# Optimization experiments

Hardware: AMD Instinct MI355X
Metric: run time of the kernel (lower is better)

The kernel has to match this reference:

```python
import jax, jax.numpy as jnp
import numpy as np

NUM_EMBEDDINGS = 1024
EMBEDDING_DIM = 64
COMMITMENT_COST = 0.25


def setup_inputs() -> dict:
    key = jax.random.key(0)
    k_x, k_cb = jax.random.split(key)
    x = jax.random.normal(k_x, (16, EMBEDDING_DIM, 64, 64), dtype=jnp.float32)
    # nn.Embedding weight init: uniform(-1/K, 1/K)
    codebook = jax.random.uniform(
        k_cb, (NUM_EMBEDDINGS, EMBEDDING_DIM), dtype=jnp.float32,
        minval=-1.0 / NUM_EMBEDDINGS, maxval=1.0 / NUM_EMBEDDINGS)
    return {"x": x, "codebook": codebook}


def reference(x, codebook):
    sg = jax.lax.stop_gradient
    # NCHW -> NHWC
    inputs = jnp.transpose(x, (0, 2, 3, 1))  # [B,H,W,D]
    in_shape = inputs.shape
    flat = inputs.reshape(-1, EMBEDDING_DIM)  # [N,D]
    # squared L2 distances to each codebook entry: [N,K]
    distances = (jnp.sum(flat ** 2, axis=1, keepdims=True)
                 + jnp.sum(codebook ** 2, axis=1)
                 - 2.0 * jnp.matmul(flat, codebook.T))
    encoding_indices = jnp.argmin(distances, axis=1)  # [N]
    # one-hot matmul in the original == plain gather
    quantized = codebook[encoding_indices].reshape(in_shape)  # [B,H,W,D]
    e_latent_loss = jnp.mean((sg(quantized) - inputs) ** 2)
    q_latent_loss = jnp.mean((quantized - sg(inputs)) ** 2)
    loss = q_latent_loss + COMMITMENT_COST * e_latent_loss
    # straight-through estimator
    quantized = inputs + sg(quantized - inputs)
    quantized = jnp.transpose(quantized, (0, 3, 1, 2))  # NHWC -> NCHW
    return quantized, loss
```

## Files before the change

### kernel.cpp

```cpp
#include <hip/hip_runtime.h>

#define NPTS   65536
#define DIM    64
#define KCODES 1024
#define HW     4096
#define CH     128
#define NCH    8
#define ROWP   72

typedef __attribute__((ext_vector_type(8))) short  short8;
typedef __attribute__((ext_vector_type(4))) float  floatx4;

__device__ __forceinline__ short f2bf(float f) {
    unsigned u = __builtin_bit_cast(unsigned, f);
    u = (u + 0x7FFFu + ((u >> 16) & 1u)) >> 16;
    return (short)u;
}

__global__ __launch_bounds__(512, 4) void vq_fused(
    const float* __restrict__ x, const float* __restrict__ cb,
    float* __restrict__ out, float* __restrict__ loss_ptr)
{
    __shared__ __align__(16) short s_cb[CH * ROWP];
    __shared__ float s_cbn[CH];
    __shared__ float s_part[2][128];
    __shared__ float s_xn[128];
    __shared__ float s_red[2];

    const int tid  = threadIdx.x;
    const int lane = tid & 63;
    const int wave = tid >> 6;
    const int col  = lane & 15;
    const int quad = lane >> 4;
    const int pg   = wave & 3;
    const int kc   = wave >> 2;

    const int pb = blockIdx.x * 128 + pg * 32;
    short8 afrag[2][2];
    #pragma unroll
    for (int pt = 0; pt < 2; ++pt) {
        int n = pb + pt * 16 + col;
        const float* bp = x + ((size_t)(n >> 12) << 18) + (n & 4095);
        float ns = 0.0f;
        #pragma unroll
        for (int kh = 0; kh < 2; ++kh) {
            short8 f;
            #pragma unroll
            for (int j = 0; j < 8; ++j) {
                float v = bp[(size_t)(kh * 32 + quad * 8 + j) * HW];
                f[j] = f2bf(v);
                ns = fmaf(v, v, ns);
            }
            afrag[pt][kh] = f;
        }
        ns += __shfl_xor(ns, 16, 64);
        ns += __shfl_xor(ns, 32, 64);
        if (kc == 0 && quad == 0) s_xn[pg * 32 + pt * 16 + col] = ns;
    }

    float best[2][4];
    #pragma unroll
    for (int pt = 0; pt < 2; ++pt)
        #pragma unroll
        for (int r = 0; r < 4; ++r) best[pt][r] = -3.4e38f;

    for (int c = 0; c < NCH; ++c) {
        __syncthreads();
        #pragma unroll
        for (int i = 0; i < 2; ++i) {
            int g = tid + 512 * i;
            const float4* p4 = (const float4*)cb + (size_t)c * 2048 + 2 * g;
            float4 va = p4[0], vb = p4[1];
            short8 v;
            v[0] = f2bf(va.x); v[1] = f2bf(va.y); v[2] = f2bf(va.z); v[3] = f2bf(va.w);
            v[4] = f2bf(vb.x); v[5] = f2bf(vb.y); v[6] = f2bf(vb.z); v[7] = f2bf(vb.w);
            int cc = g >> 3, part = g & 7;
            *(short8*)&s_cb[cc * ROWP + part * 8] = v;
            float ns = fmaf(va.x, va.x, fmaf(va.y, va.y, fmaf(va.z, va.z, va.w * va.w)));
            ns = fmaf(vb.x, vb.x, fmaf(vb.y, vb.y, fmaf(vb.z, vb.z, fmaf(vb.w, vb.w, ns))));
            ns += __shfl_xor(ns, 1, 64);
            ns += __shfl_xor(ns, 2, 64);
            ns += __shfl_xor(ns, 4, 64);
            if ((tid & 7) == 0) s_cbn[cc] = -0.5f * ns;
        }
        __syncthreads();
        #pragma unroll
        for (int ct = 0; ct < 4; ++ct) {
            int cc = kc * 64 + ct * 16 + col;
            float initv = s_cbn[cc];
            unsigned idxv = (unsigned)(c * CH + cc);
            const short* rp = &s_cb[cc * ROWP + quad * 8];
            short8 b0 = *(const short8*)rp;
            short8 b1 = *(const short8*)(rp + 32);
            floatx4 cinit = {initv, initv, initv, initv};
            #pragma unroll
            for (int pt = 0; pt < 2; ++pt) {
                floatx4 acc = __builtin_amdgcn_mfma_f32_16x16x32_bf16(afrag[pt][0], b0, cinit, 0, 0, 0);
                acc = __builtin_amdgcn_mfma_f32_16x16x32_bf16(afrag[pt][1], b1, acc, 0, 0, 0);
                #pragma unroll
                for (int r = 0; r < 4; ++r) {
                    unsigned pbits = (__builtin_bit_cast(unsigned, acc[r]) & 0xFFFFFC00u) | idxv;
                    best[pt][r] = fmaxf(best[pt][r], __builtin_bit_cast(float, pbits));
                }
            }
        }
    }

    #pragma unroll
    for (int pt = 0; pt < 2; ++pt)
        #pragma unroll
        for (int r = 0; r < 4; ++r) {
            float v = best[pt][r];
            v = fmaxf(v, __shfl_xor(v, 1, 64));
            v = fmaxf(v, __shfl_xor(v, 2, 64));
            v = fmaxf(v, __shfl_xor(v, 4, 64));
            v = fmaxf(v, __shfl_xor(v, 8, 64));
            best[pt][r] = v;
        }
    if (col == 0) {
        #pragma unroll
        for (int pt = 0; pt < 2; ++pt)
            #pragma unroll
            for (int r = 0; r < 4; ++r)
                s_part[kc][pg * 32 + pt * 16 + quad * 4 + r] = best[pt][r];
    }
    __syncthreads();

    {
        int ptid = tid & 127;
        int dq   = tid >> 7;
        float m = fmaxf(s_part[0][ptid], s_part[1][ptid]);
        unsigned mu = __builtin_bit_cast(unsigned, m);
        int idx = (int)(mu & 1023u);
        int n = blockIdx.x * 128 + ptid;
        float* op = out + ((size_t)(n >> 12) << 18) + (n & 4095);
        const float4* crow = (const float4*)(cb + (size_t)idx * DIM + dq * 16);
        #pragma unroll
        for (int j = 0; j < 4; ++j) {
            float4 v = crow[j];
            op[(size_t)(dq * 16 + j * 4 + 0) * HW] = v.x;
            op[(size_t)(dq * 16 + j * 4 + 1) * HW] = v.y;
            op[(size_t)(dq * 16 + j * 4 + 2) * HW] = v.z;
            op[(size_t)(dq * 16 + j * 4 + 3) * HW] = v.w;
        }
        if (dq == 0) {
            float vtr = __builtin_bit_cast(float, mu & 0xFFFFFC00u);
            float lp = s_xn[ptid] - 2.0f * vtr;
            #pragma unroll
            for (int off = 32; off > 0; off >>= 1)
                lp += __shfl_down(lp, off, 64);
            if (lane == 0) s_red[wave] = lp;
        }
    }
    __syncthreads();
    if (tid == 0)
        atomicAdd(loss_ptr, (s_red[0] + s_red[1]) * (1.25f / ((float)NPTS * DIM)));
}

extern "C" void kernel_launch(void* const* d_in, const int* in_sizes, int n_in,
                              void* d_out, int out_size, void* d_ws, size_t ws_size,
                              hipStream_t stream) {
    const float* x  = (const float*)d_in[0];
    const float* cb = (const float*)d_in[1];
    float* out      = (float*)d_out;
    float* loss_ptr = out + (size_t)NPTS * DIM;

    vq_fused<<<NPTS / 128, 512, 0, stream>>>(x, cb, out, loss_ptr);
}
```

Before: 90.17 us.

## Double-buffer codebook chunks with register prefetch and shrink blocks to 64 points

Codebook chunks are now staged through registers: the next chunk's global loads are issued before the barrier, and shared memory is double-buffered, which removes one barrier per iteration and overlaps load latency with MFMA work. Blocks shrink from 512 threads covering 128 points to 256 threads covering 64 points, giving twice as many blocks. The loss is reduced with one atomic per wave instead of a block-level reduction. In exchange, each block converts the full codebook for only half as many points, so codebook traffic and bf16 conversion work per point double. Register pressure also rises and atomic contention on the loss grows.

```diff
diff --git a/kernel.cpp b/kernel.cpp
--- a/kernel.cpp
+++ b/kernel.cpp
@@ -17,25 +17,32 @@
     return (short)u;
 }
 
-__global__ __launch_bounds__(512, 4) void vq_fused(
+__global__ __launch_bounds__(256) void vq_fused(
     const float* __restrict__ x, const float* __restrict__ cb,
     float* __restrict__ out, float* __restrict__ loss_ptr)
 {
-    __shared__ __align__(16) short s_cb[CH * ROWP];
-    __shared__ float s_cbn[CH];
-    __shared__ float s_part[2][128];
-    __shared__ float s_xn[128];
-    __shared__ float s_red[2];
+    __shared__ __align__(16) short s_cb[2][CH * ROWP];
+    __shared__ float s_cbn[2][CH];
+    __shared__ float s_part[2][64];
+    __shared__ float s_xn[64];
 
     const int tid  = threadIdx.x;
     const int lane = tid & 63;
     const int wave = tid >> 6;
     const int col  = lane & 15;
     const int quad = lane >> 4;
-    const int pg   = wave & 3;
-    const int kc   = wave >> 2;
+    const int pg   = wave & 1;
+    const int kc   = wave >> 1;
 
-    const int pb = blockIdx.x * 128 + pg * 32;
+    float4 st[8];
+    #pragma unroll
+    for (int i = 0; i < 4; ++i) {
+        const float4* p4 = (const float4*)cb + 2 * (tid + 256 * i);
+        st[2 * i]     = p4[0];
+        st[2 * i + 1] = p4[1];
+    }
+
+    const int pb = blockIdx.x * 64 + pg * 32;
     short8 afrag[2][2];
     #pragma unroll
     for (int pt = 0; pt < 2; ++pt) {
@@ -65,31 +72,39 @@
         for (int r = 0; r < 4; ++r) best[pt][r] = -3.4e38f;
 
     for (int c = 0; c < NCH; ++c) {
-        __syncthreads();
+        const int buf = c & 1;
         #pragma unroll
-        for (int i = 0; i < 2; ++i) {
-            int g = tid + 512 * i;
-            const float4* p4 = (const float4*)cb + (size_t)c * 2048 + 2 * g;
-            float4 va = p4[0], vb = p4[1];
+        for (int i = 0; i < 4; ++i) {
+            float4 va = st[2 * i], vb = st[2 * i + 1];
             short8 v;
             v[0] = f2bf(va.x); v[1] = f2bf(va.y); v[2] = f2bf(va.z); v[3] = f2bf(va.w);
             v[4] = f2bf(vb.x); v[5] = f2bf(vb.y); v[6] = f2bf(vb.z); v[7] = f2bf(vb.w);
+            int g = tid + 256 * i;
             int cc = g >> 3, part = g & 7;
-            *(short8*)&s_cb[cc * ROWP + part * 8] = v;
+            *(short8*)&s_cb[buf][cc * ROWP + part * 8] = v;
             float ns = fmaf(va.x, va.x, fmaf(va.y, va.y, fmaf(va.z, va.z, va.w * va.w)));
             ns = fmaf(vb.x, vb.x, fmaf(vb.y, vb.y, fmaf(vb.z, vb.z, fmaf(vb.w, vb.w, ns))));
             ns += __shfl_xor(ns, 1, 64);
             ns += __shfl_xor(ns, 2, 64);
             ns += __shfl_xor(ns, 4, 64);
-            if ((tid & 7) == 0) s_cbn[cc] = -0.5f * ns;
+            if ((tid & 7) == 0) s_cbn[buf][cc] = -0.5f * ns;
+        }
+        if (c < NCH - 1) {
+            #pragma unroll
+            for (int i = 0; i < 4; ++i) {
+                const float4* p4 = (const float4*)cb + (size_t)(c + 1) * 2048
+                                   + 2 * (tid + 256 * i);
+                st[2 * i]     = p4[0];
+                st[2 * i + 1] = p4[1];
+            }
         }
         __syncthreads();
         #pragma unroll
         for (int ct = 0; ct < 4; ++ct) {
             int cc = kc * 64 + ct * 16 + col;
-            float initv = s_cbn[cc];
+            float initv = s_cbn[buf][cc];
             unsigned idxv = (unsigned)(c * CH + cc);
-            const short* rp = &s_cb[cc * ROWP + quad * 8];
+            const short* rp = &s_cb[buf][cc * ROWP + quad * 8];
             short8 b0 = *(const short8*)rp;
             short8 b1 = *(const short8*)(rp + 32);
             floatx4 cinit = {initv, initv, initv, initv};
@@ -127,12 +142,12 @@
     __syncthreads();
 
     {
-        int ptid = tid & 127;
-        int dq   = tid >> 7;
+        int ptid = lane;
+        int dq   = wave;
         float m = fmaxf(s_part[0][ptid], s_part[1][ptid]);
         unsigned mu = __builtin_bit_cast(unsigned, m);
         int idx = (int)(mu & 1023u);
-        int n = blockIdx.x * 128 + ptid;
+        int n = blockIdx.x * 64 + ptid;
         float* op = out + ((size_t)(n >> 12) << 18) + (n & 4095);
         const float4* crow = (const float4*)(cb + (size_t)idx * DIM + dq * 16);
         #pragma unroll
@@ -149,12 +164,10 @@
             #pragma unroll
             for (int off = 32; off > 0; off >>= 1)
                 lp += __shfl_down(lp, off, 64);
-            if (lane == 0) s_red[wave] = lp;
+            if (lane == 0)
+                atomicAdd(loss_ptr, lp * (1.25f / ((float)NPTS * DIM)));
         }
     }
-    __syncthreads();
-    if (tid == 0)
-        atomicAdd(loss_ptr, (s_red[0] + s_red[1]) * (1.25f / ((float)NPTS * DIM)));
 }
 
 extern "C" void kernel_launch(void* const* d_in, const int* in_sizes, int n_in,
@@ -165,5 +178,5 @@
     float* out      = (float*)d_out;
     float* loss_ptr = out + (size_t)NPTS * DIM;
 
-    vq_fused<<<NPTS / 128, 512, 0, stream>>>(x, cb, out, loss_ptr);
+    vq_fused<<<NPTS / 64, 256, 0, stream>>>(x, cb, out, loss_ptr);
 }
```

Result: slower. 94.41 us (+4.7%).

## Split VQ into score kernel and coalesced emit kernel with deterministic loss

Applied to the files above, without the earlier changes.

The fused kernel is split in two. The first kernel computes argmin-packed scores per point and per-block loss partials into workspace. The second kernel, one block per (batch, channel), stages a codebook column in LDS and writes the output with coalesced vector stores, replacing the strided per-channel scatter of the old epilogue. It also reduces the loss partials without atomics. The cost is a second launch and an extra round trip of the score array through workspace.

```diff
diff --git a/kernel.cpp b/kernel.cpp
--- a/kernel.cpp
+++ b/kernel.cpp
@@ -17,9 +17,9 @@
     return (short)u;
 }
 
-__global__ __launch_bounds__(512, 4) void vq_fused(
+__global__ __launch_bounds__(512, 4) void vq_score(
     const float* __restrict__ x, const float* __restrict__ cb,
-    float* __restrict__ out, float* __restrict__ loss_ptr)
+    float* __restrict__ ps, float* __restrict__ partials)
 {
     __shared__ __align__(16) short s_cb[CH * ROWP];
     __shared__ float s_cbn[CH];
@@ -69,15 +69,15 @@
         #pragma unroll
         for (int i = 0; i < 2; ++i) {
             int g = tid + 512 * i;
-            const float4* p4 = (const float4*)cb + (size_t)c * 2048 + 2 * g;
-            float4 va = p4[0], vb = p4[1];
+            const floatx4* p4 = (const floatx4*)cb + (size_t)c * 2048 + 2 * g;
+            floatx4 va = p4[0], vb = p4[1];
             short8 v;
-            v[0] = f2bf(va.x); v[1] = f2bf(va.y); v[2] = f2bf(va.z); v[3] = f2bf(va.w);
-            v[4] = f2bf(vb.x); v[5] = f2bf(vb.y); v[6] = f2bf(vb.z); v[7] = f2bf(vb.w);
+            v[0] = f2bf(va[0]); v[1] = f2bf(va[1]); v[2] = f2bf(va[2]); v[3] = f2bf(va[3]);
+            v[4] = f2bf(vb[0]); v[5] = f2bf(vb[1]); v[6] = f2bf(vb[2]); v[7] = f2bf(vb[3]);
             int cc = g >> 3, part = g & 7;
             *(short8*)&s_cb[cc * ROWP + part * 8] = v;
-            float ns = fmaf(va.x, va.x, fmaf(va.y, va.y, fmaf(va.z, va.z, va.w * va.w)));
-            ns = fmaf(vb.x, vb.x, fmaf(vb.y, vb.y, fmaf(vb.z, vb.z, fmaf(vb.w, vb.w, ns))));
+            float ns = fmaf(va[0], va[0], fmaf(va[1], va[1], fmaf(va[2], va[2], va[3] * va[3])));
+            ns = fmaf(vb[0], vb[0], fmaf(vb[1], vb[1], fmaf(vb[2], vb[2], fmaf(vb[3], vb[3], ns))));
             ns += __shfl_xor(ns, 1, 64);
             ns += __shfl_xor(ns, 2, 64);
             ns += __shfl_xor(ns, 4, 64);
@@ -126,35 +126,64 @@
     }
     __syncthreads();
 
-    {
-        int ptid = tid & 127;
-        int dq   = tid >> 7;
-        float m = fmaxf(s_part[0][ptid], s_part[1][ptid]);
+    if (tid < 128) {
+        float m = fmaxf(s_part[0][tid], s_part[1][tid]);
+        ps[blockIdx.x * 128 + tid] = m;
         unsigned mu = __builtin_bit_cast(unsigned, m);
-        int idx = (int)(mu & 1023u);
-        int n = blockIdx.x * 128 + ptid;
-        float* op = out + ((size_t)(n >> 12) << 18) + (n & 4095);
-        const float4* crow = (const float4*)(cb + (size_t)idx * DIM + dq * 16);
-        #pragma unroll
-        for (int j = 0; j < 4; ++j) {
-            float4 v = crow[j];
-            op[(size_t)(dq * 16 + j * 4 + 0) * HW] = v.x;
-            op[(size_t)(dq * 16 + j * 4 + 1) * HW] = v.y;
-            op[(size_t)(dq * 16 + j * 4 + 2) * HW] = v.z;
-            op[(size_t)(dq * 16 + j * 4 + 3) * HW] = v.w;
-        }
-        if (dq == 0) {
-            float vtr = __builtin_bit_cast(float, mu & 0xFFFFFC00u);
-            float lp = s_xn[ptid] - 2.0f * vtr;
-            #pragma unroll
-            for (int off = 32; off > 0; off >>= 1)
-                lp += __shfl_down(lp, off, 64);
-            if (lane == 0) s_red[wave] = lp;
-        }
+        float vtr = __builtin_bit_cast(float, mu & 0xFFFFFC00u);
+        float lp = s_xn[tid] - 2.0f * vtr;
+        #pragma unroll
+        for (int off = 32; off > 0; off >>= 1)
+            lp += __shfl_down(lp, off, 64);
+        if (lane == 0) s_red[wave] = lp;
     }
     __syncthreads();
-    if (tid == 0)
-        atomicAdd(loss_ptr, (s_red[0] + s_red[1]) * (1.25f / ((float)NPTS * DIM)));
+    if (tid == 0) partials[blockIdx.x] = s_red[0] + s_red[1];
+}
+
+__global__ __launch_bounds__(256) void vq_emit(
+    const float* __restrict__ cb, const float* __restrict__ ps,
+    const float* __restrict__ partials, float* __restrict__ out,
+    float* __restrict__ loss_ptr)
+{
+    __shared__ float s_col[KCODES];
+    __shared__ float s_lred[4];
+
+    const int tid = threadIdx.x;
+    const int B   = blockIdx.x;
+    const int d   = B & 63;
+    const int b   = B >> 6;
+
+    #pragma unroll
+    for (int i = 0; i < 4; ++i)
+        s_col[tid + 256 * i] = cb[(size_t)(tid + 256 * i) * DIM + d];
+    __syncthreads();
+
+    const floatx4* psp = (const floatx4*)(ps + (size_t)b * HW) + tid * 4;
+    floatx4* op = (floatx4*)(out + (size_t)B * HW) + tid * 4;
+    #pragma unroll
+    for (int i = 0; i < 4; ++i) {
+        floatx4 pv = psp[i];
+        floatx4 ov;
+        #pragma unroll
+        for (int e = 0; e < 4; ++e) {
+            unsigned idx = __builtin_bit_cast(unsigned, pv[e]) & 1023u;
+            ov[e] = s_col[idx];
+        }
+        op[i] = ov;
+    }
+
+    if (B == 0) {
+        float s = partials[tid] + partials[tid + 256];
+        #pragma unroll
+        for (int off = 32; off > 0; off >>= 1)
+            s += __shfl_down(s, off, 64);
+        if ((tid & 63) == 0) s_lred[tid >> 6] = s;
+        __syncthreads();
+        if (tid == 0)
+            *loss_ptr = (s_lred[0] + s_lred[1] + s_lred[2] + s_lred[3])
+                        * (1.25f / ((float)NPTS * DIM));
+    }
 }
 
 extern "C" void kernel_launch(void* const* d_in, const int* in_sizes, int n_in,
@@ -165,5 +194,9 @@
     float* out      = (float*)d_out;
     float* loss_ptr = out + (size_t)NPTS * DIM;
 
-    vq_fused<<<NPTS / 128, 512, 0, stream>>>(x, cb, out, loss_ptr);
-}
+    float* ps       = (float*)d_ws;
+    float* partials = ps + NPTS;
+
+    vq_score<<<NPTS / 128, 512, 0, stream>>>(x, cb, ps, partials);
+    vq_emit<<<(NPTS * DIM) / (256 * 16), 256, 0, stream>>>(cb, ps, partials, out, loss_ptr);
+}
```

Result: slower. 95.38 us (+5.8%).
